# Kernel tuning notes

Hardware: AMD Instinct MI355X
Metric: run time of the kernel (lower is better)

The kernel has to match this reference:

```python
import jax, jax.numpy as jnp
import numpy as np

HEADS = 8


def setup_inputs() -> dict:
    key = jax.random.key(0)
    k0, k1, k2, k3 = jax.random.split(key, 4)
    N, C_in, T = 4, 256, 2048
    C_kq, C_out = 512, 512
    x = jax.random.normal(k0, (N, C_in, T), dtype=jnp.float32)
    # Conv1d(kernel_size=1, bias=False) weights squeezed to (out, in)
    Wq = jax.random.normal(k1, (C_kq, C_in), dtype=jnp.float32) * 0.02
    Wk = jax.random.normal(k2, (C_kq, C_in), dtype=jnp.float32) * 0.02
    Wv = jax.random.normal(k3, (C_out, C_in), dtype=jnp.float32) * 0.02
    return {"x": x, "Wq": Wq, "Wk": Wk, "Wv": Wv}


def reference(x, Wq, Wk, Wv):
    N, C, T = x.shape
    H = HEADS
    C_kq = Wq.shape[0]
    C_out = Wv.shape[0]
    dk = C_kq // H
    dv = C_out // H
    # 1x1 conv == per-timestep linear projection
    q = jnp.einsum('oc,nct->not', Wq, x).reshape(N, H, dk, T)
    k = jnp.einsum('oc,nct->not', Wk, x).reshape(N, H, dk, T)
    v = jnp.einsum('oc,nct->not', Wv, x).reshape(N, H, dv, T)
    scale = 1.0 / np.sqrt(dk)
    # scores[n,h,tk,tq] = sum_d q[n,h,d,tq] * k[n,h,d,tk]
    scores = jnp.einsum('nhdq,nhdk->nhkq', q, k) * scale
    attn = jax.nn.softmax(scores, axis=2)  # softmax over key axis tk
    # out[n,h,d,tq] = sum_tk attn[n,h,tk,tq] * v[n,h,d,tk]
    out = jnp.einsum('nhkq,nhdk->nhdq', attn, v)
    return out.reshape(N, C_out, T)
```

## Files before the change

kernel.cpp:

```cpp
#include <hip/hip_runtime.h>
#include <stdint.h>

#define T_SEQ 2048
#define CIN 256
#define COUT 512
#define NHEAD 8
#define DH 64
#define LROW 72

typedef __bf16 bf16x8 __attribute__((ext_vector_type(8)));
typedef float f32x4 __attribute__((ext_vector_type(4)));
typedef float f32x16 __attribute__((ext_vector_type(16)));
typedef unsigned short u16x8 __attribute__((ext_vector_type(8)));
typedef unsigned u32x4 __attribute__((ext_vector_type(4)));

static __device__ __forceinline__ unsigned short bf16_rne(float f) {
  unsigned u = __builtin_bit_cast(unsigned, f);
  u += 0x7FFFu + ((u >> 16) & 1u);
  return (unsigned short)(u >> 16);
}

static __device__ __forceinline__ unsigned cvt_pk_bf16(float lo, float hi) {
  unsigned r;
  asm("v_cvt_pk_bf16_f32 %0, %1, %2" : "=v"(r) : "v"(lo), "v"(hi));
  return r;
}

static __device__ __forceinline__ void plswap(unsigned& a, unsigned& b) {
  auto rr = __builtin_amdgcn_permlane32_swap((int)a, (int)b, false, false);
  a = (unsigned)rr[0];
  b = (unsigned)rr[1];
}

static __device__ __forceinline__ bf16x8 ld_frag(const unsigned short* p) {
  u16x8 v = *(const u16x8*)p;
  return __builtin_bit_cast(bf16x8, v);
}

__global__ __launch_bounds__(256) void pack_w_k(const float* __restrict__ wq,
                                                const float* __restrict__ wk,
                                                const float* __restrict__ wv,
                                                unsigned short* __restrict__ wb) {
  int i = blockIdx.x * 256 + threadIdx.x;
  const float* src = (i < 131072) ? wq : (i < 262144) ? wk : wv;
  wb[i] = bf16_rne(src[i & 131071]);
}

__global__ __launch_bounds__(256) void pack_xT_k(const float* __restrict__ x,
                                                 unsigned short* __restrict__ xT) {
  __shared__ float tile[64][65];
  const int n = blockIdx.z, c0 = blockIdx.y * 64, t0 = blockIdx.x * 64;
  const int i = threadIdx.x;
  {
    const int cc = i >> 2, tch = (i & 3) * 16;
    const float* src = x + ((size_t)n * CIN + c0 + cc) * T_SEQ + t0 + tch;
    const float4* s4 = (const float4*)src;
#pragma unroll
    for (int q = 0; q < 4; ++q) {
      float4 v = s4[q];
      tile[cc][tch + q * 4 + 0] = v.x;
      tile[cc][tch + q * 4 + 1] = v.y;
      tile[cc][tch + q * 4 + 2] = v.z;
      tile[cc][tch + q * 4 + 3] = v.w;
    }
  }
  __syncthreads();
  {
    const int tt = i >> 2, cch = (i & 3) * 16;
    unsigned short* dst = xT + ((size_t)n * T_SEQ + t0 + tt) * CIN + c0 + cch;
    u16x8 w0, w1;
#pragma unroll
    for (int j = 0; j < 8; ++j) w0[j] = bf16_rne(tile[cch + j][tt]);
#pragma unroll
    for (int j = 0; j < 8; ++j) w1[j] = bf16_rne(tile[cch + 8 + j][tt]);
    *(u16x8*)dst = w0;
    *(u16x8*)(dst + 8) = w1;
  }
}

__global__ __launch_bounds__(256) void proj_k(const unsigned short* __restrict__ wb,
                                              const unsigned short* __restrict__ xT,
                                              unsigned short* __restrict__ qb,
                                              unsigned short* __restrict__ kb,
                                              unsigned short* __restrict__ vb) {
  __shared__ unsigned short vt_lds[64][136];
  const int n = blockIdx.z;
  const unsigned short* X = xT + (size_t)n * T_SEQ * CIN;
  const int tid = threadIdx.x, wave = tid >> 6, lane = tid & 63;
  const int c = lane & 15, g = lane >> 4;
  const int o0 = blockIdx.x * 64;
  const int t0 = blockIdx.y * 128 + wave * 32;

  bf16x8 a[8][2];
#pragma unroll
  for (int k8 = 0; k8 < 8; ++k8)
#pragma unroll
    for (int mt = 0; mt < 2; ++mt)
      a[k8][mt] = ld_frag(X + (size_t)(t0 + mt * 16 + c) * CIN + k8 * 32 + g * 8);

  const f32x4 z4 = {0.f, 0.f, 0.f, 0.f};
  const int h = o0 >> 6;
  const size_t base = ((size_t)(n * NHEAD + h)) * T_SEQ * DH;

  for (int w = 0; w < 3; ++w) {
    const unsigned short* W = wb + (size_t)w * COUT * CIN;
    f32x4 acc[2][4];
#pragma unroll
    for (int mt = 0; mt < 2; ++mt)
#pragma unroll
      for (int no = 0; no < 4; ++no) acc[mt][no] = z4;

#pragma unroll
    for (int k8 = 0; k8 < 8; ++k8) {
      bf16x8 b[4];
#pragma unroll
      for (int no = 0; no < 4; ++no)
        b[no] = ld_frag(W + (size_t)(o0 + no * 16 + c) * CIN + k8 * 32 + g * 8);
#pragma unroll
      for (int mt = 0; mt < 2; ++mt)
#pragma unroll
        for (int no = 0; no < 4; ++no)
          acc[mt][no] = __builtin_amdgcn_mfma_f32_16x16x32_bf16(a[k8][mt], b[no], acc[mt][no], 0, 0, 0);
    }

    if (w == 2) {
#pragma unroll
      for (int mt = 0; mt < 2; ++mt)
#pragma unroll
        for (int no = 0; no < 4; ++no) {
          const int d = no * 16 + c;
          const int lt = (wave * 32) + mt * 16 + 4 * g;
#pragma unroll
          for (int pr = 0; pr < 2; ++pr) {
            const unsigned pw = (unsigned)bf16_rne(acc[mt][no][2 * pr]) |
                                ((unsigned)bf16_rne(acc[mt][no][2 * pr + 1]) << 16);
            *(unsigned*)&vt_lds[d][lt + 2 * pr] = pw;
          }
        }
      __syncthreads();
      const int row = tid >> 2, seg = tid & 3;
      unsigned short* dst = vb + base + (size_t)row * T_SEQ + blockIdx.y * 128 + seg * 32;
      const unsigned short* srcl = &vt_lds[row][seg * 32];
#pragma unroll
      for (int q = 0; q < 4; ++q) *(u16x8*)(dst + q * 8) = *(const u16x8*)(srcl + q * 8);
    } else {
      unsigned short* dst = (w == 0) ? qb : kb;
      const float scale = (w == 0) ? 0.18033688011112043f : 1.0f;
#pragma unroll
      for (int mt = 0; mt < 2; ++mt)
#pragma unroll
        for (int no = 0; no < 4; ++no)
#pragma unroll
          for (int r = 0; r < 4; ++r) {
            const int t = t0 + mt * 16 + 4 * g + r;
            const int d = no * 16 + c;
            dst[base + (size_t)t * DH + d] = bf16_rne(acc[mt][no][r] * scale);
          }
    }
  }
}

__global__ __launch_bounds__(512) void attn_k(const unsigned short* __restrict__ qb,
                                              const unsigned short* __restrict__ kb,
                                              const unsigned short* __restrict__ vbt,
                                              float* __restrict__ outp) {
  __shared__ unsigned short smem[4 * 2 * 4608];

  const int bid = blockIdx.x;
  const int sid = (bid & 7) * 32 + (bid >> 3);
  const int tqt = sid & 7, nh = sid >> 3;

  const int tid = threadIdx.x;
  const int wave = tid >> 6, lane = tid & 63;
  const int half = wave >> 2;
  const int ln = lane & 31, hi = lane >> 5;
  const int tq0 = tqt * 256 + (wave & 3) * 64;
  const unsigned short* Q = qb + (size_t)nh * T_SEQ * DH;
  const unsigned short* K = kb + (size_t)nh * T_SEQ * DH;
  const unsigned short* V = vbt + (size_t)nh * T_SEQ * DH;

  bf16x8 qf0[4], qf1[4];
#pragma unroll
  for (int dblk = 0; dblk < 4; ++dblk) {
    qf0[dblk] = ld_frag(Q + (size_t)(tq0 + ln) * DH + dblk * 16 + hi * 8);
    qf1[dblk] = ld_frag(Q + (size_t)(tq0 + 32 + ln) * DH + dblk * 16 + hi * 8);
  }

  const f32x16 z16 = {0.f, 0.f, 0.f, 0.f, 0.f, 0.f, 0.f, 0.f,
                      0.f, 0.f, 0.f, 0.f, 0.f, 0.f, 0.f, 0.f};
  f32x16 oacc00 = z16, oacc01 = z16;
  f32x16 oacc10 = z16, oacc11 = z16;
  float l_run0 = 0.f, l_run1 = 0.f;

  const int ht = tid & 255;
  const int srow = ht & 63, sseg = ht >> 6;
  const unsigned short* kseg = K + (size_t)(half * 1024 + srow) * DH + sseg * 16;
  const unsigned short* vseg = V + (size_t)srow * T_SEQ + half * 1024 + sseg * 16;
  const int swoff = srow * LROW + sseg * 16;
  const int row0 = ln * LROW;
  const int row1 = (32 + ln) * LROW;
  const int hioff = hi * 8;

  unsigned short* krb = smem + half * 18432;
  unsigned short* kab = krb + 4608;
  unsigned short* vrb = krb + 9216;
  unsigned short* vab = krb + 13824;
  {
    u16x8 k0 = *(const u16x8*)kseg;
    u16x8 k1 = *(const u16x8*)(kseg + 8);
    u16x8 v0 = *(const u16x8*)vseg;
    u16x8 v1 = *(const u16x8*)(vseg + 8);
    *(u16x8*)&krb[swoff] = k0;
    *(u16x8*)&krb[swoff + 8] = k1;
    *(u16x8*)&vrb[swoff] = v0;
    *(u16x8*)&vrb[swoff + 8] = v1;
  }
  __syncthreads();

  const int NT2 = T_SEQ / 64 / 2;
  for (int t = 0; t < NT2; ++t) {
    const bool pre = (t + 1 < NT2);
    u16x8 kn0, kn1, vn0, vn1;
    if (pre) {
      const unsigned short* ks = kseg + (size_t)(t + 1) * (64 * DH);
      kn0 = *(const u16x8*)ks;
      kn1 = *(const u16x8*)(ks + 8);
      const unsigned short* vs = vseg + (size_t)(t + 1) * 64;
      vn0 = *(const u16x8*)vs;
      vn1 = *(const u16x8*)(vs + 8);
    }
    f32x16 sa00 = z16, sa01 = z16, sa10 = z16, sa11 = z16;
    __builtin_amdgcn_s_setprio(1);
#pragma unroll
    for (int dblk = 0; dblk < 4; ++dblk) {
      bf16x8 ka0 = ld_frag(krb + row0 + dblk * 16 + hioff);
      bf16x8 ka1 = ld_frag(krb + row1 + dblk * 16 + hioff);
      sa00 = __builtin_amdgcn_mfma_f32_32x32x16_bf16(ka0, qf0[dblk], sa00, 0, 0, 0);
      sa01 = __builtin_amdgcn_mfma_f32_32x32x16_bf16(ka1, qf0[dblk], sa01, 0, 0, 0);
      sa10 = __builtin_amdgcn_mfma_f32_32x32x16_bf16(ka0, qf1[dblk], sa10, 0, 0, 0);
      sa11 = __builtin_amdgcn_mfma_f32_32x32x16_bf16(ka1, qf1[dblk], sa11, 0, 0, 0);
    }
    __builtin_amdgcn_s_setprio(0);
    bf16x8 pa0[4], pa1[4];
    {
      float p0[16], p1[16];
      float cs = 0.f;
#pragma unroll
      for (int r = 0; r < 16; ++r) {
        p0[r] = __builtin_amdgcn_exp2f(sa00[r]);
        p1[r] = __builtin_amdgcn_exp2f(sa01[r]);
        cs += p0[r] + p1[r];
      }
      cs += __shfl_xor(cs, 32);
      l_run0 += cs;
      unsigned W0[8], W1[8];
#pragma unroll
      for (int j = 0; j < 8; ++j) {
        W0[j] = cvt_pk_bf16(p0[2 * j], p0[2 * j + 1]);
        W1[j] = cvt_pk_bf16(p1[2 * j], p1[2 * j + 1]);
      }
      plswap(W0[0], W0[2]); plswap(W0[1], W0[3]);
      plswap(W0[4], W0[6]); plswap(W0[5], W0[7]);
      plswap(W1[0], W1[2]); plswap(W1[1], W1[3]);
      plswap(W1[4], W1[6]); plswap(W1[5], W1[7]);
      u32x4 f;
      f[0] = W0[0]; f[1] = W0[1]; f[2] = W0[2]; f[3] = W0[3];
      pa0[0] = __builtin_bit_cast(bf16x8, f);
      f[0] = W0[4]; f[1] = W0[5]; f[2] = W0[6]; f[3] = W0[7];
      pa0[1] = __builtin_bit_cast(bf16x8, f);
      f[0] = W1[0]; f[1] = W1[1]; f[2] = W1[2]; f[3] = W1[3];
      pa0[2] = __builtin_bit_cast(bf16x8, f);
      f[0] = W1[4]; f[1] = W1[5]; f[2] = W1[6]; f[3] = W1[7];
      pa0[3] = __builtin_bit_cast(bf16x8, f);
    }
    {
      float p0[16], p1[16];
      float cs = 0.f;
#pragma unroll
      for (int r = 0; r < 16; ++r) {
        p0[r] = __builtin_amdgcn_exp2f(sa10[r]);
        p1[r] = __builtin_amdgcn_exp2f(sa11[r]);
        cs += p0[r] + p1[r];
      }
      cs += __shfl_xor(cs, 32);
      l_run1 += cs;
      unsigned W0[8], W1[8];
#pragma unroll
      for (int j = 0; j < 8; ++j) {
        W0[j] = cvt_pk_bf16(p0[2 * j], p0[2 * j + 1]);
        W1[j] = cvt_pk_bf16(p1[2 * j], p1[2 * j + 1]);
      }
      plswap(W0[0], W0[2]); plswap(W0[1], W0[3]);
      plswap(W0[4], W0[6]); plswap(W0[5], W0[7]);
      plswap(W1[0], W1[2]); plswap(W1[1], W1[3]);
      plswap(W1[4], W1[6]); plswap(W1[5], W1[7]);
      u32x4 f;
      f[0] = W0[0]; f[1] = W0[1]; f[2] = W0[2]; f[3] = W0[3];
      pa1[0] = __builtin_bit_cast(bf16x8, f);
      f[0] = W0[4]; f[1] = W0[5]; f[2] = W0[6]; f[3] = W0[7];
      pa1[1] = __builtin_bit_cast(bf16x8, f);
      f[0] = W1[0]; f[1] = W1[1]; f[2] = W1[2]; f[3] = W1[3];
      pa1[2] = __builtin_bit_cast(bf16x8, f);
      f[0] = W1[4]; f[1] = W1[5]; f[2] = W1[6]; f[3] = W1[7];
      pa1[3] = __builtin_bit_cast(bf16x8, f);
    }
    __builtin_amdgcn_s_setprio(1);
#pragma unroll
    for (int kbk = 0; kbk < 4; ++kbk) {
      bf16x8 vf0 = ld_frag(vrb + row0 + kbk * 16 + hioff);
      bf16x8 vf1 = ld_frag(vrb + row1 + kbk * 16 + hioff);
      oacc00 = __builtin_amdgcn_mfma_f32_32x32x16_bf16(pa0[kbk], vf0, oacc00, 0, 0, 0);
      oacc01 = __builtin_amdgcn_mfma_f32_32x32x16_bf16(pa0[kbk], vf1, oacc01, 0, 0, 0);
      oacc10 = __builtin_amdgcn_mfma_f32_32x32x16_bf16(pa1[kbk], vf0, oacc10, 0, 0, 0);
      oacc11 = __builtin_amdgcn_mfma_f32_32x32x16_bf16(pa1[kbk], vf1, oacc11, 0, 0, 0);
    }
    __builtin_amdgcn_s_setprio(0);
    if (pre) {
      *(u16x8*)&kab[swoff] = kn0;
      *(u16x8*)&kab[swoff + 8] = kn1;
      *(u16x8*)&vab[swoff] = vn0;
      *(u16x8*)&vab[swoff + 8] = vn1;
    }
    __syncthreads();
    unsigned short* tp;
    tp = krb; krb = kab; kab = tp;
    tp = vrb; vrb = vab; vab = tp;
  }

  float* mbuf = (float*)smem;
  const int MS = 4224;
  if (half == 1) {
    float* mb = mbuf + (wave - 4) * MS;
#pragma unroll
    for (int r = 0; r < 16; ++r) mb[r * 64 + lane] = oacc00[r];
#pragma unroll
    for (int r = 0; r < 16; ++r) mb[1024 + r * 64 + lane] = oacc01[r];
#pragma unroll
    for (int r = 0; r < 16; ++r) mb[2048 + r * 64 + lane] = oacc10[r];
#pragma unroll
    for (int r = 0; r < 16; ++r) mb[3072 + r * 64 + lane] = oacc11[r];
    mb[4096 + lane] = l_run0;
    mb[4160 + lane] = l_run1;
  }
  __syncthreads();
  if (half == 0) {
    float* mb = mbuf + wave * MS;
#pragma unroll
    for (int r = 0; r < 16; ++r) oacc00[r] += mb[r * 64 + lane];
#pragma unroll
    for (int r = 0; r < 16; ++r) oacc01[r] += mb[1024 + r * 64 + lane];
#pragma unroll
    for (int r = 0; r < 16; ++r) oacc10[r] += mb[2048 + r * 64 + lane];
#pragma unroll
    for (int r = 0; r < 16; ++r) oacc11[r] += mb[3072 + r * 64 + lane];
    l_run0 += mb[4096 + lane];
    l_run1 += mb[4160 + lane];

    const int n = nh >> 3, h = nh & 7;
    const size_t obase = (size_t)(n * COUT + h * DH) * T_SEQ;
    const int d0 = ln, d1 = 32 + ln;
#pragma unroll
    for (int rq = 0; rq < 4; ++rq) {
      const int tbase = tq0 + 8 * rq + 4 * hi;
      f32x4 o0, o1, o2, o3;
#pragma unroll
      for (int j = 0; j < 4; ++j) {
        const float lv0 = __shfl(l_run0, 8 * rq + 4 * hi + j);
        const float inv0 = __builtin_amdgcn_rcpf(lv0);
        const float lv1 = __shfl(l_run1, 8 * rq + 4 * hi + j);
        const float inv1 = __builtin_amdgcn_rcpf(lv1);
        o0[j] = oacc00[4 * rq + j] * inv0;
        o1[j] = oacc01[4 * rq + j] * inv0;
        o2[j] = oacc10[4 * rq + j] * inv1;
        o3[j] = oacc11[4 * rq + j] * inv1;
      }
      *(f32x4*)&outp[obase + (size_t)d0 * T_SEQ + tbase] = o0;
      *(f32x4*)&outp[obase + (size_t)d1 * T_SEQ + tbase] = o1;
      *(f32x4*)&outp[obase + (size_t)d0 * T_SEQ + tbase + 32] = o2;
      *(f32x4*)&outp[obase + (size_t)d1 * T_SEQ + tbase + 32] = o3;
    }
  }
}

extern "C" void kernel_launch(void* const* d_in, const int* in_sizes, int n_in,
                              void* d_out, int out_size, void* d_ws, size_t ws_size,
                              hipStream_t stream) {
  (void)in_sizes; (void)n_in; (void)out_size; (void)ws_size;
  const float* x  = (const float*)d_in[0];
  const float* Wq = (const float*)d_in[1];
  const float* Wk = (const float*)d_in[2];
  const float* Wv = (const float*)d_in[3];
  float* outp = (float*)d_out;

  char* ws = (char*)d_ws;
  unsigned short* wb = (unsigned short*)ws;
  unsigned short* xT = (unsigned short*)(ws + 786432);
  unsigned short* qb = (unsigned short*)(ws + 4980736);
  unsigned short* kb = qb + 4194304;
  unsigned short* vb = kb + 4194304;

  pack_w_k<<<1536, 256, 0, stream>>>(Wq, Wk, Wv, wb);
  pack_xT_k<<<dim3(32, 4, 4), 256, 0, stream>>>(x, xT);
  proj_k<<<dim3(8, 16, 4), 256, 0, stream>>>(wb, xT, qb, kb, vb);
  attn_k<<<256, 512, 0, stream>>>(qb, kb, vb, outp);
}
```

Measured before the change: 87.22 us.

## Software-pipeline QK^T across tiles, drop split-K halves, merge pack kernels

The attention kernel no longer splits the key range across two half-blocks of 4 waves with a final shared-memory reduction. It now runs 256 threads that walk all 64 key tiles, computing the next tile's QK^T scores before the current tile's softmax and PV step. K and V loads are staggered across double buffers to hide latency. The two packing kernels are merged into one launch to save a launch. The trade-off is half as many waves per block, so there is less parallelism per CU, plus extra register pressure from holding two score sets.

```diff
diff --git a/kernel.cpp b/kernel.cpp
--- a/kernel.cpp
+++ b/kernel.cpp
@@ -37,20 +37,23 @@
   return __builtin_bit_cast(bf16x8, v);
 }
 
-__global__ __launch_bounds__(256) void pack_w_k(const float* __restrict__ wq,
-                                                const float* __restrict__ wk,
-                                                const float* __restrict__ wv,
-                                                unsigned short* __restrict__ wb) {
-  int i = blockIdx.x * 256 + threadIdx.x;
-  const float* src = (i < 131072) ? wq : (i < 262144) ? wk : wv;
-  wb[i] = bf16_rne(src[i & 131071]);
-}
-
-__global__ __launch_bounds__(256) void pack_xT_k(const float* __restrict__ x,
-                                                 unsigned short* __restrict__ xT) {
+__global__ __launch_bounds__(256) void pack_k(const float* __restrict__ x,
+                                              const float* __restrict__ wq,
+                                              const float* __restrict__ wk,
+                                              const float* __restrict__ wv,
+                                              unsigned short* __restrict__ wb,
+                                              unsigned short* __restrict__ xT) {
   __shared__ float tile[64][65];
-  const int n = blockIdx.z, c0 = blockIdx.y * 64, t0 = blockIdx.x * 64;
+  const int b = blockIdx.x;
   const int i = threadIdx.x;
+  if (b < 1536) {
+    const int idx = b * 256 + i;
+    const float* src = (idx < 131072) ? wq : (idx < 262144) ? wk : wv;
+    wb[idx] = bf16_rne(src[idx & 131071]);
+    return;
+  }
+  const int b2 = b - 1536;
+  const int t0 = (b2 & 31) * 64, c0 = ((b2 >> 5) & 3) * 64, n = b2 >> 7;
   {
     const int cc = i >> 2, tch = (i & 3) * 16;
     const float* src = x + ((size_t)n * CIN + c0 + cc) * T_SEQ + t0 + tch;
@@ -160,21 +163,25 @@
   }
 }
 
-__global__ __launch_bounds__(512) void attn_k(const unsigned short* __restrict__ qb,
+__global__ __launch_bounds__(256) void attn_k(const unsigned short* __restrict__ qb,
                                               const unsigned short* __restrict__ kb,
                                               const unsigned short* __restrict__ vbt,
                                               float* __restrict__ outp) {
-  __shared__ unsigned short smem[4 * 2 * 4608];
+  __shared__ unsigned short smem[4 * 4608];
+  unsigned short* kA = smem;
+  unsigned short* kB = smem + 4608;
+  unsigned short* vA = smem + 9216;
+  unsigned short* vB = smem + 13824;
 
   const int bid = blockIdx.x;
   const int sid = (bid & 7) * 32 + (bid >> 3);
   const int tqt = sid & 7, nh = sid >> 3;
 
   const int tid = threadIdx.x;
-  const int wave = tid >> 6, lane = tid & 63;
-  const int half = wave >> 2;
+  const int lane = tid & 63;
+  const int wave = tid >> 6;
   const int ln = lane & 31, hi = lane >> 5;
-  const int tq0 = tqt * 256 + (wave & 3) * 64;
+  const int tq0 = tqt * 256 + wave * 64;
   const unsigned short* Q = qb + (size_t)nh * T_SEQ * DH;
   const unsigned short* K = kb + (size_t)nh * T_SEQ * DH;
   const unsigned short* V = vbt + (size_t)nh * T_SEQ * DH;
@@ -188,76 +195,105 @@
 
   const f32x16 z16 = {0.f, 0.f, 0.f, 0.f, 0.f, 0.f, 0.f, 0.f,
                       0.f, 0.f, 0.f, 0.f, 0.f, 0.f, 0.f, 0.f};
-  f32x16 oacc00 = z16, oacc01 = z16;
-  f32x16 oacc10 = z16, oacc11 = z16;
+  f32x16 oacc00 = z16, oacc01 = z16, oacc10 = z16, oacc11 = z16;
   float l_run0 = 0.f, l_run1 = 0.f;
 
-  const int ht = tid & 255;
-  const int srow = ht & 63, sseg = ht >> 6;
-  const unsigned short* kseg = K + (size_t)(half * 1024 + srow) * DH + sseg * 16;
-  const unsigned short* vseg = V + (size_t)srow * T_SEQ + half * 1024 + sseg * 16;
+  const int srow = tid & 63, sseg = tid >> 6;
+  const unsigned short* kseg = K + (size_t)srow * DH + sseg * 16;
+  const unsigned short* vseg = V + (size_t)srow * T_SEQ + sseg * 16;
   const int swoff = srow * LROW + sseg * 16;
   const int row0 = ln * LROW;
   const int row1 = (32 + ln) * LROW;
   const int hioff = hi * 8;
 
-  unsigned short* krb = smem + half * 18432;
-  unsigned short* kab = krb + 4608;
-  unsigned short* vrb = krb + 9216;
-  unsigned short* vab = krb + 13824;
+  const int NT = T_SEQ / 64;
+  u16x8 kn0, kn1, vn0, vn1;
+
   {
-    u16x8 k0 = *(const u16x8*)kseg;
-    u16x8 k1 = *(const u16x8*)(kseg + 8);
-    u16x8 v0 = *(const u16x8*)vseg;
-    u16x8 v1 = *(const u16x8*)(vseg + 8);
-    *(u16x8*)&krb[swoff] = k0;
-    *(u16x8*)&krb[swoff + 8] = k1;
-    *(u16x8*)&vrb[swoff] = v0;
-    *(u16x8*)&vrb[swoff + 8] = v1;
+    u16x8 a0 = *(const u16x8*)kseg;
+    u16x8 a1 = *(const u16x8*)(kseg + 8);
+    u16x8 b0 = *(const u16x8*)vseg;
+    u16x8 b1 = *(const u16x8*)(vseg + 8);
+    *(u16x8*)&kA[swoff] = a0;
+    *(u16x8*)&kA[swoff + 8] = a1;
+    *(u16x8*)&vA[swoff] = b0;
+    *(u16x8*)&vA[swoff + 8] = b1;
+    kn0 = *(const u16x8*)(kseg + 64 * DH);
+    kn1 = *(const u16x8*)(kseg + 64 * DH + 8);
   }
   __syncthreads();
 
-  const int NT2 = T_SEQ / 64 / 2;
-  for (int t = 0; t < NT2; ++t) {
-    const bool pre = (t + 1 < NT2);
-    u16x8 kn0, kn1, vn0, vn1;
-    if (pre) {
-      const unsigned short* ks = kseg + (size_t)(t + 1) * (64 * DH);
-      kn0 = *(const u16x8*)ks;
-      kn1 = *(const u16x8*)(ks + 8);
-      const unsigned short* vs = vseg + (size_t)(t + 1) * 64;
-      vn0 = *(const u16x8*)vs;
-      vn1 = *(const u16x8*)(vs + 8);
-    }
-    f32x16 sa00 = z16, sa01 = z16, sa10 = z16, sa11 = z16;
+  f32x16 sa[4], sb[4];
+  {
     __builtin_amdgcn_s_setprio(1);
 #pragma unroll
     for (int dblk = 0; dblk < 4; ++dblk) {
-      bf16x8 ka0 = ld_frag(krb + row0 + dblk * 16 + hioff);
-      bf16x8 ka1 = ld_frag(krb + row1 + dblk * 16 + hioff);
-      sa00 = __builtin_amdgcn_mfma_f32_32x32x16_bf16(ka0, qf0[dblk], sa00, 0, 0, 0);
-      sa01 = __builtin_amdgcn_mfma_f32_32x32x16_bf16(ka1, qf0[dblk], sa01, 0, 0, 0);
-      sa10 = __builtin_amdgcn_mfma_f32_32x32x16_bf16(ka0, qf1[dblk], sa10, 0, 0, 0);
-      sa11 = __builtin_amdgcn_mfma_f32_32x32x16_bf16(ka1, qf1[dblk], sa11, 0, 0, 0);
+      bf16x8 ka0 = ld_frag(kA + row0 + dblk * 16 + hioff);
+      bf16x8 ka1 = ld_frag(kA + row1 + dblk * 16 + hioff);
+      sa[0] = __builtin_amdgcn_mfma_f32_32x32x16_bf16(ka0, qf0[dblk], (dblk == 0) ? z16 : sa[0], 0, 0, 0);
+      sa[1] = __builtin_amdgcn_mfma_f32_32x32x16_bf16(ka1, qf0[dblk], (dblk == 0) ? z16 : sa[1], 0, 0, 0);
+      sa[2] = __builtin_amdgcn_mfma_f32_32x32x16_bf16(ka0, qf1[dblk], (dblk == 0) ? z16 : sa[2], 0, 0, 0);
+      sa[3] = __builtin_amdgcn_mfma_f32_32x32x16_bf16(ka1, qf1[dblk], (dblk == 0) ? z16 : sa[3], 0, 0, 0);
     }
     __builtin_amdgcn_s_setprio(0);
+  }
+  *(u16x8*)&kB[swoff] = kn0;
+  *(u16x8*)&kB[swoff + 8] = kn1;
+  kn0 = *(const u16x8*)(kseg + 2 * 64 * DH);
+  kn1 = *(const u16x8*)(kseg + 2 * 64 * DH + 8);
+  vn0 = *(const u16x8*)(vseg + 64);
+  vn1 = *(const u16x8*)(vseg + 64 + 8);
+  __syncthreads();
+
+  auto body = [&](int t, f32x16 (&sc)[4], f32x16 (&sn)[4],
+                  unsigned short* krd, unsigned short* kwr,
+                  unsigned short* vrd, unsigned short* vwr) {
+    const bool qn = (t + 1 < NT);
+    if (qn) {
+      __builtin_amdgcn_s_setprio(1);
+#pragma unroll
+      for (int dblk = 0; dblk < 4; ++dblk) {
+        bf16x8 ka0 = ld_frag(krd + row0 + dblk * 16 + hioff);
+        bf16x8 ka1 = ld_frag(krd + row1 + dblk * 16 + hioff);
+        sn[0] = __builtin_amdgcn_mfma_f32_32x32x16_bf16(ka0, qf0[dblk], (dblk == 0) ? z16 : sn[0], 0, 0, 0);
+        sn[1] = __builtin_amdgcn_mfma_f32_32x32x16_bf16(ka1, qf0[dblk], (dblk == 0) ? z16 : sn[1], 0, 0, 0);
+        sn[2] = __builtin_amdgcn_mfma_f32_32x32x16_bf16(ka0, qf1[dblk], (dblk == 0) ? z16 : sn[2], 0, 0, 0);
+        sn[3] = __builtin_amdgcn_mfma_f32_32x32x16_bf16(ka1, qf1[dblk], (dblk == 0) ? z16 : sn[3], 0, 0, 0);
+      }
+      __builtin_amdgcn_s_setprio(0);
+    }
+    if (t + 1 < NT) {
+      *(u16x8*)&vwr[swoff] = vn0;
+      *(u16x8*)&vwr[swoff + 8] = vn1;
+    }
+    if (t + 2 < NT) {
+      *(u16x8*)&kwr[swoff] = kn0;
+      *(u16x8*)&kwr[swoff + 8] = kn1;
+    }
+    if (t + 2 < NT) {
+      vn0 = *(const u16x8*)(vseg + (size_t)(t + 2) * 64);
+      vn1 = *(const u16x8*)(vseg + (size_t)(t + 2) * 64 + 8);
+    }
+    if (t + 3 < NT) {
+      kn0 = *(const u16x8*)(kseg + (size_t)(t + 3) * (64 * DH));
+      kn1 = *(const u16x8*)(kseg + (size_t)(t + 3) * (64 * DH) + 8);
+    }
     bf16x8 pa0[4], pa1[4];
     {
-      float p0[16], p1[16];
       float cs = 0.f;
 #pragma unroll
       for (int r = 0; r < 16; ++r) {
-        p0[r] = __builtin_amdgcn_exp2f(sa00[r]);
-        p1[r] = __builtin_amdgcn_exp2f(sa01[r]);
-        cs += p0[r] + p1[r];
+        sc[0][r] = __builtin_amdgcn_exp2f(sc[0][r]);
+        sc[1][r] = __builtin_amdgcn_exp2f(sc[1][r]);
+        cs += sc[0][r] + sc[1][r];
       }
       cs += __shfl_xor(cs, 32);
       l_run0 += cs;
       unsigned W0[8], W1[8];
 #pragma unroll
       for (int j = 0; j < 8; ++j) {
-        W0[j] = cvt_pk_bf16(p0[2 * j], p0[2 * j + 1]);
-        W1[j] = cvt_pk_bf16(p1[2 * j], p1[2 * j + 1]);
+        W0[j] = cvt_pk_bf16(sc[0][2 * j], sc[0][2 * j + 1]);
+        W1[j] = cvt_pk_bf16(sc[1][2 * j], sc[1][2 * j + 1]);
       }
       plswap(W0[0], W0[2]); plswap(W0[1], W0[3]);
       plswap(W0[4], W0[6]); plswap(W0[5], W0[7]);
@@ -274,21 +310,20 @@
       pa0[3] = __builtin_bit_cast(bf16x8, f);
     }
     {
-      float p0[16], p1[16];
       float cs = 0.f;
 #pragma unroll
       for (int r = 0; r < 16; ++r) {
-        p0[r] = __builtin_amdgcn_exp2f(sa10[r]);
-        p1[r] = __builtin_amdgcn_exp2f(sa11[r]);
-        cs += p0[r] + p1[r];
+        sc[2][r] = __builtin_amdgcn_exp2f(sc[2][r]);
+        sc[3][r] = __builtin_amdgcn_exp2f(sc[3][r]);
+        cs += sc[2][r] + sc[3][r];
       }
       cs += __shfl_xor(cs, 32);
       l_run1 += cs;
       unsigned W0[8], W1[8];
 #pragma unroll
       for (int j = 0; j < 8; ++j) {
-        W0[j] = cvt_pk_bf16(p0[2 * j], p0[2 * j + 1]);
-        W1[j] = cvt_pk_bf16(p1[2 * j], p1[2 * j + 1]);
+        W0[j] = cvt_pk_bf16(sc[2][2 * j], sc[2][2 * j + 1]);
+        W1[j] = cvt_pk_bf16(sc[3][2 * j], sc[3][2 * j + 1]);
       }
       plswap(W0[0], W0[2]); plswap(W0[1], W0[3]);
       plswap(W0[4], W0[6]); plswap(W0[5], W0[7]);
@@ -307,78 +342,44 @@
     __builtin_amdgcn_s_setprio(1);
 #pragma unroll
     for (int kbk = 0; kbk < 4; ++kbk) {
-      bf16x8 vf0 = ld_frag(vrb + row0 + kbk * 16 + hioff);
-      bf16x8 vf1 = ld_frag(vrb + row1 + kbk * 16 + hioff);
+      bf16x8 vf0 = ld_frag(vrd + row0 + kbk * 16 + hioff);
+      bf16x8 vf1 = ld_frag(vrd + row1 + kbk * 16 + hioff);
       oacc00 = __builtin_amdgcn_mfma_f32_32x32x16_bf16(pa0[kbk], vf0, oacc00, 0, 0, 0);
       oacc01 = __builtin_amdgcn_mfma_f32_32x32x16_bf16(pa0[kbk], vf1, oacc01, 0, 0, 0);
       oacc10 = __builtin_amdgcn_mfma_f32_32x32x16_bf16(pa1[kbk], vf0, oacc10, 0, 0, 0);
       oacc11 = __builtin_amdgcn_mfma_f32_32x32x16_bf16(pa1[kbk], vf1, oacc11, 0, 0, 0);
     }
     __builtin_amdgcn_s_setprio(0);
-    if (pre) {
-      *(u16x8*)&kab[swoff] = kn0;
-      *(u16x8*)&kab[swoff + 8] = kn1;
-      *(u16x8*)&vab[swoff] = vn0;
-      *(u16x8*)&vab[swoff + 8] = vn1;
-    }
     __syncthreads();
-    unsigned short* tp;
-    tp = krb; krb = kab; kab = tp;
-    tp = vrb; vrb = vab; vab = tp;
-  }
-
-  float* mbuf = (float*)smem;
-  const int MS = 4224;
-  if (half == 1) {
-    float* mb = mbuf + (wave - 4) * MS;
-#pragma unroll
-    for (int r = 0; r < 16; ++r) mb[r * 64 + lane] = oacc00[r];
-#pragma unroll
-    for (int r = 0; r < 16; ++r) mb[1024 + r * 64 + lane] = oacc01[r];
-#pragma unroll
-    for (int r = 0; r < 16; ++r) mb[2048 + r * 64 + lane] = oacc10[r];
-#pragma unroll
-    for (int r = 0; r < 16; ++r) mb[3072 + r * 64 + lane] = oacc11[r];
-    mb[4096 + lane] = l_run0;
-    mb[4160 + lane] = l_run1;
-  }
-  __syncthreads();
-  if (half == 0) {
-    float* mb = mbuf + wave * MS;
-#pragma unroll
-    for (int r = 0; r < 16; ++r) oacc00[r] += mb[r * 64 + lane];
-#pragma unroll
-    for (int r = 0; r < 16; ++r) oacc01[r] += mb[1024 + r * 64 + lane];
-#pragma unroll
-    for (int r = 0; r < 16; ++r) oacc10[r] += mb[2048 + r * 64 + lane];
-#pragma unroll
-    for (int r = 0; r < 16; ++r) oacc11[r] += mb[3072 + r * 64 + lane];
-    l_run0 += mb[4096 + lane];
-    l_run1 += mb[4160 + lane];
-
-    const int n = nh >> 3, h = nh & 7;
-    const size_t obase = (size_t)(n * COUT + h * DH) * T_SEQ;
-    const int d0 = ln, d1 = 32 + ln;
-#pragma unroll
-    for (int rq = 0; rq < 4; ++rq) {
-      const int tbase = tq0 + 8 * rq + 4 * hi;
-      f32x4 o0, o1, o2, o3;
-#pragma unroll
-      for (int j = 0; j < 4; ++j) {
-        const float lv0 = __shfl(l_run0, 8 * rq + 4 * hi + j);
-        const float inv0 = __builtin_amdgcn_rcpf(lv0);
-        const float lv1 = __shfl(l_run1, 8 * rq + 4 * hi + j);
-        const float inv1 = __builtin_amdgcn_rcpf(lv1);
-        o0[j] = oacc00[4 * rq + j] * inv0;
-        o1[j] = oacc01[4 * rq + j] * inv0;
-        o2[j] = oacc10[4 * rq + j] * inv1;
-        o3[j] = oacc11[4 * rq + j] * inv1;
-      }
-      *(f32x4*)&outp[obase + (size_t)d0 * T_SEQ + tbase] = o0;
-      *(f32x4*)&outp[obase + (size_t)d1 * T_SEQ + tbase] = o1;
-      *(f32x4*)&outp[obase + (size_t)d0 * T_SEQ + tbase + 32] = o2;
-      *(f32x4*)&outp[obase + (size_t)d1 * T_SEQ + tbase + 32] = o3;
-    }
+  };
+
+  for (int tt = 0; tt < NT; tt += 2) {
+    body(tt, sa, sb, kB, kA, vA, vB);
+    body(tt + 1, sb, sa, kA, kB, vB, vA);
+  }
+
+  const int n = nh >> 3, h = nh & 7;
+  const size_t obase = (size_t)(n * COUT + h * DH) * T_SEQ;
+  const int d0 = ln, d1 = 32 + ln;
+#pragma unroll
+  for (int rq = 0; rq < 4; ++rq) {
+    const int tbase = tq0 + 8 * rq + 4 * hi;
+    f32x4 o0, o1, o2, o3;
+#pragma unroll
+    for (int j = 0; j < 4; ++j) {
+      const float lv0 = __shfl(l_run0, 8 * rq + 4 * hi + j);
+      const float inv0 = __builtin_amdgcn_rcpf(lv0);
+      const float lv1 = __shfl(l_run1, 8 * rq + 4 * hi + j);
+      const float inv1 = __builtin_amdgcn_rcpf(lv1);
+      o0[j] = oacc00[4 * rq + j] * inv0;
+      o1[j] = oacc01[4 * rq + j] * inv0;
+      o2[j] = oacc10[4 * rq + j] * inv1;
+      o3[j] = oacc11[4 * rq + j] * inv1;
+    }
+    *(f32x4*)&outp[obase + (size_t)d0 * T_SEQ + tbase] = o0;
+    *(f32x4*)&outp[obase + (size_t)d1 * T_SEQ + tbase] = o1;
+    *(f32x4*)&outp[obase + (size_t)d0 * T_SEQ + tbase + 32] = o2;
+    *(f32x4*)&outp[obase + (size_t)d1 * T_SEQ + tbase + 32] = o3;
   }
 }
 
@@ -399,8 +400,7 @@
   unsigned short* kb = qb + 4194304;
   unsigned short* vb = kb + 4194304;
 
-  pack_w_k<<<1536, 256, 0, stream>>>(Wq, Wk, Wv, wb);
-  pack_xT_k<<<dim3(32, 4, 4), 256, 0, stream>>>(x, xT);
+  pack_k<<<2048, 256, 0, stream>>>(x, Wq, Wk, Wv, wb, xT);
   proj_k<<<dim3(8, 16, 4), 256, 0, stream>>>(wb, xT, qb, kb, vb);
-  attn_k<<<256, 512, 0, stream>>>(qb, kb, vb, outp);
-}
+  attn_k<<<256, 256, 0, stream>>>(qb, kb, vb, outp);
+}
```

Result: slower. 89.94 us (+3.1%).

## Split attention key range four ways per block and merge pack kernels

Applied to the files above, without the earlier changes.

The attention kernel now launches 1024 threads per block and splits the key sequence into four quarters instead of two. Each quarter has its own double-buffered K/V shared-memory region, and the partial accumulators are reduced in two stages through shared memory. Separately, the weight and x-transpose pack kernels are merged into one launch to remove a kernel launch. The aim is more waves per CU to hide latency in the attention loop, at the cost of twice the shared memory per block, higher register pressure under the 1024-thread bound, and a longer reduction tail.

```diff
diff --git a/kernel.cpp b/kernel.cpp
--- a/kernel.cpp
+++ b/kernel.cpp
@@ -37,20 +37,23 @@
   return __builtin_bit_cast(bf16x8, v);
 }
 
-__global__ __launch_bounds__(256) void pack_w_k(const float* __restrict__ wq,
-                                                const float* __restrict__ wk,
-                                                const float* __restrict__ wv,
-                                                unsigned short* __restrict__ wb) {
-  int i = blockIdx.x * 256 + threadIdx.x;
-  const float* src = (i < 131072) ? wq : (i < 262144) ? wk : wv;
-  wb[i] = bf16_rne(src[i & 131071]);
-}
-
-__global__ __launch_bounds__(256) void pack_xT_k(const float* __restrict__ x,
-                                                 unsigned short* __restrict__ xT) {
+__global__ __launch_bounds__(256) void pack_k(const float* __restrict__ x,
+                                              const float* __restrict__ wq,
+                                              const float* __restrict__ wk,
+                                              const float* __restrict__ wv,
+                                              unsigned short* __restrict__ wb,
+                                              unsigned short* __restrict__ xT) {
   __shared__ float tile[64][65];
-  const int n = blockIdx.z, c0 = blockIdx.y * 64, t0 = blockIdx.x * 64;
+  const int b = blockIdx.x;
   const int i = threadIdx.x;
+  if (b < 1536) {
+    const int idx = b * 256 + i;
+    const float* src = (idx < 131072) ? wq : (idx < 262144) ? wk : wv;
+    wb[idx] = bf16_rne(src[idx & 131071]);
+    return;
+  }
+  const int b2 = b - 1536;
+  const int t0 = (b2 & 31) * 64, c0 = ((b2 >> 5) & 3) * 64, n = b2 >> 7;
   {
     const int cc = i >> 2, tch = (i & 3) * 16;
     const float* src = x + ((size_t)n * CIN + c0 + cc) * T_SEQ + t0 + tch;
@@ -160,11 +163,11 @@
   }
 }
 
-__global__ __launch_bounds__(512) void attn_k(const unsigned short* __restrict__ qb,
-                                              const unsigned short* __restrict__ kb,
-                                              const unsigned short* __restrict__ vbt,
-                                              float* __restrict__ outp) {
-  __shared__ unsigned short smem[4 * 2 * 4608];
+__global__ __launch_bounds__(1024) void attn_k(const unsigned short* __restrict__ qb,
+                                               const unsigned short* __restrict__ kb,
+                                               const unsigned short* __restrict__ vbt,
+                                               float* __restrict__ outp) {
+  __shared__ unsigned short smem[4 * 4 * 4608];
 
   const int bid = blockIdx.x;
   const int sid = (bid & 7) * 32 + (bid >> 3);
@@ -172,9 +175,10 @@
 
   const int tid = threadIdx.x;
   const int wave = tid >> 6, lane = tid & 63;
-  const int half = wave >> 2;
+  const int quarter = wave >> 2;
+  const int wq4 = wave & 3;
   const int ln = lane & 31, hi = lane >> 5;
-  const int tq0 = tqt * 256 + (wave & 3) * 64;
+  const int tq0 = tqt * 256 + wq4 * 64;
   const unsigned short* Q = qb + (size_t)nh * T_SEQ * DH;
   const unsigned short* K = kb + (size_t)nh * T_SEQ * DH;
   const unsigned short* V = vbt + (size_t)nh * T_SEQ * DH;
@@ -194,14 +198,14 @@
 
   const int ht = tid & 255;
   const int srow = ht & 63, sseg = ht >> 6;
-  const unsigned short* kseg = K + (size_t)(half * 1024 + srow) * DH + sseg * 16;
-  const unsigned short* vseg = V + (size_t)srow * T_SEQ + half * 1024 + sseg * 16;
+  const unsigned short* kseg = K + (size_t)(quarter * 512 + srow) * DH + sseg * 16;
+  const unsigned short* vseg = V + (size_t)srow * T_SEQ + quarter * 512 + sseg * 16;
   const int swoff = srow * LROW + sseg * 16;
   const int row0 = ln * LROW;
   const int row1 = (32 + ln) * LROW;
   const int hioff = hi * 8;
 
-  unsigned short* krb = smem + half * 18432;
+  unsigned short* krb = smem + quarter * 18432;
   unsigned short* kab = krb + 4608;
   unsigned short* vrb = krb + 9216;
   unsigned short* vab = krb + 13824;
@@ -217,9 +221,9 @@
   }
   __syncthreads();
 
-  const int NT2 = T_SEQ / 64 / 2;
-  for (int t = 0; t < NT2; ++t) {
-    const bool pre = (t + 1 < NT2);
+  const int NT4 = T_SEQ / 64 / 4;
+  for (int t = 0; t < NT4; ++t) {
+    const bool pre = (t + 1 < NT4);
     u16x8 kn0, kn1, vn0, vn1;
     if (pre) {
       const unsigned short* ks = kseg + (size_t)(t + 1) * (64 * DH);
@@ -329,8 +333,8 @@
 
   float* mbuf = (float*)smem;
   const int MS = 4224;
-  if (half == 1) {
-    float* mb = mbuf + (wave - 4) * MS;
+  if (quarter == 1 || quarter == 2) {
+    float* mb = mbuf + ((quarter - 1) * 4 + wq4) * MS;
 #pragma unroll
     for (int r = 0; r < 16; ++r) mb[r * 64 + lane] = oacc00[r];
 #pragma unroll
@@ -343,8 +347,39 @@
     mb[4160 + lane] = l_run1;
   }
   __syncthreads();
-  if (half == 0) {
-    float* mb = mbuf + wave * MS;
+  if (quarter == 0) {
+#pragma unroll
+    for (int qq = 0; qq < 2; ++qq) {
+      float* mb = mbuf + (qq * 4 + wq4) * MS;
+#pragma unroll
+      for (int r = 0; r < 16; ++r) oacc00[r] += mb[r * 64 + lane];
+#pragma unroll
+      for (int r = 0; r < 16; ++r) oacc01[r] += mb[1024 + r * 64 + lane];
+#pragma unroll
+      for (int r = 0; r < 16; ++r) oacc10[r] += mb[2048 + r * 64 + lane];
+#pragma unroll
+      for (int r = 0; r < 16; ++r) oacc11[r] += mb[3072 + r * 64 + lane];
+      l_run0 += mb[4096 + lane];
+      l_run1 += mb[4160 + lane];
+    }
+  }
+  __syncthreads();
+  if (quarter == 3) {
+    float* mb = mbuf + wq4 * MS;
+#pragma unroll
+    for (int r = 0; r < 16; ++r) mb[r * 64 + lane] = oacc00[r];
+#pragma unroll
+    for (int r = 0; r < 16; ++r) mb[1024 + r * 64 + lane] = oacc01[r];
+#pragma unroll
+    for (int r = 0; r < 16; ++r) mb[2048 + r * 64 + lane] = oacc10[r];
+#pragma unroll
+    for (int r = 0; r < 16; ++r) mb[3072 + r * 64 + lane] = oacc11[r];
+    mb[4096 + lane] = l_run0;
+    mb[4160 + lane] = l_run1;
+  }
+  __syncthreads();
+  if (quarter == 0) {
+    float* mb = mbuf + wq4 * MS;
 #pragma unroll
     for (int r = 0; r < 16; ++r) oacc00[r] += mb[r * 64 + lane];
 #pragma unroll
@@ -399,8 +434,7 @@
   unsigned short* kb = qb + 4194304;
   unsigned short* vb = kb + 4194304;
 
-  pack_w_k<<<1536, 256, 0, stream>>>(Wq, Wk, Wv, wb);
-  pack_xT_k<<<dim3(32, 4, 4), 256, 0, stream>>>(x, xT);
+  pack_k<<<2048, 256, 0, stream>>>(x, Wq, Wk, Wv, wb, xT);
   proj_k<<<dim3(8, 16, 4), 256, 0, stream>>>(wb, xT, qb, kb, vb);
-  attn_k<<<256, 512, 0, stream>>>(qb, kb, vb, outp);
-}
+  attn_k<<<256, 1024, 0, stream>>>(qb, kb, vb, outp);
+}
```

New measurement: 299.6 us. 243% more time.
